# Performance work log

Measured on AMD Instinct MI355X. Metric: run time of the kernel, lower is better.

The kernel has to match this reference:

```python
import jax, jax.numpy as jnp
import numpy as np

L = 1024            # sequence length (env states fed as inputs_embeds)
D_IN = 4            # raw state dim
D_MODEL = 768       # mamba hidden size (mamba-130m-class backbone)
N_LAYERS = 24
D_INNER = 1536      # expand(2) * d_model
D_STATE = 16
D_CONV = 4
DT_RANK = 48        # d_model // 16
EPS = 1e-5


def setup_inputs():
    key = jax.random.key(0)
    ks = jax.random.split(key, 8)
    s = 0.02
    def nrm(k, sh, sc=s):
        return jax.random.normal(k, sh, dtype=jnp.float32) * sc
    # dt bias init: softplus^{-1}(0.01), as in Mamba reference init
    dt_bias = jnp.log(jnp.expm1(jnp.full((N_LAYERS, D_INNER), 0.01, dtype=jnp.float32)))
    # S4D-real init: A_nd = n+1
    A_log = jnp.log(jnp.broadcast_to(jnp.arange(1, D_STATE + 1, dtype=jnp.float32),
                                     (N_LAYERS, D_INNER, D_STATE)))
    return {
        "x": jax.random.normal(ks[0], (L, D_IN), dtype=jnp.float32),
        "w_enc": nrm(ks[1], (D_IN, D_MODEL), 0.5),
        "b_enc": jnp.zeros((D_MODEL,), jnp.float32),
        "norm_w": jnp.ones((N_LAYERS, D_MODEL), jnp.float32),
        "in_proj_w": nrm(ks[2], (N_LAYERS, D_MODEL, 2 * D_INNER)),
        "conv_w": nrm(ks[3], (N_LAYERS, D_INNER, D_CONV), 0.1),
        "conv_b": jnp.zeros((N_LAYERS, D_INNER), jnp.float32),
        "x_proj_w": nrm(ks[4], (N_LAYERS, D_INNER, DT_RANK + 2 * D_STATE)),
        "dt_proj_w": nrm(ks[5], (N_LAYERS, DT_RANK, D_INNER)),
        "dt_proj_b": dt_bias,
        "A_log": A_log,
        "D_skip": jnp.ones((N_LAYERS, D_INNER), jnp.float32),
        "out_proj_w": nrm(ks[6], (N_LAYERS, D_INNER, D_MODEL)),
        "norm_f_w": jnp.ones((D_MODEL,), jnp.float32),
        "fc_w": nrm(ks[7], (D_MODEL, 2), 0.05),
        "fc_b": jnp.zeros((2,), jnp.float32),
    }


def _rmsnorm(x, w):
    return x * jax.lax.rsqrt(jnp.mean(x * x, axis=-1, keepdims=True) + EPS) * w


def _mamba_block(u, p):
    # u: [L, D_MODEL]; pre-norm residual Mamba block
    norm_w, in_w, cw, cb, xp_w, dt_w, dt_b, A_log, D_skip, out_w = p
    h = _rmsnorm(u, norm_w)
    xz = h @ in_w                                   # [L, 2*D_INNER]
    xpart, z = jnp.split(xz, 2, axis=-1)
    # causal depthwise conv1d (kernel D_CONV, left-padded)
    xc = jax.lax.conv_general_dilated(
        xpart.T[None], cw[:, None, :], (1,), [(D_CONV - 1, 0)],
        feature_group_count=D_INNER)[0].T + cb      # [L, D_INNER]
    xc = jax.nn.silu(xc)
    dbl = xc @ xp_w                                 # [L, DT_RANK + 2*D_STATE]
    dt = jax.nn.softplus(dbl[:, :DT_RANK] @ dt_w + dt_b)   # [L, D_INNER]
    B = dbl[:, DT_RANK:DT_RANK + D_STATE]           # [L, D_STATE]
    C = dbl[:, DT_RANK + D_STATE:]                  # [L, D_STATE]
    A = -jnp.exp(A_log)                             # [D_INNER, D_STATE]
    dA = jnp.exp(dt[:, :, None] * A[None])          # [L, D_INNER, D_STATE]
    dBx = dt[:, :, None] * B[:, None, :] * xc[:, :, None]

    def step(hst, t):
        dA_t, dBx_t, C_t = t
        hst = dA_t * hst + dBx_t                    # [D_INNER, D_STATE]
        return hst, hst @ C_t                       # y_t: [D_INNER]

    _, ys = jax.lax.scan(step, jnp.zeros((D_INNER, D_STATE), xc.dtype), (dA, dBx, C))
    y = (ys + D_skip * xc) * jax.nn.silu(z)
    return u + y @ out_w


def reference(x, w_enc, b_enc, norm_w, in_proj_w, conv_w, conv_b, x_proj_w,
              dt_proj_w, dt_proj_b, A_log, D_skip, out_proj_w, norm_f_w, fc_w, fc_b):
    u = x @ w_enc + b_enc                           # state_encoder: [L, D_MODEL]
    params = (norm_w, in_proj_w, conv_w, conv_b, x_proj_w, dt_proj_w,
              dt_proj_b, A_log, D_skip, out_proj_w)
    block = jax.checkpoint(_mamba_block)
    u, _ = jax.lax.scan(lambda c, p: (block(c, p), None), u, params)
    u = _rmsnorm(u, norm_f_w)
    return (u[-1] @ fc_w + fc_b)[None, :]           # logits [1, 2]
```

## Files before the change

### kernel.cpp

```cpp
#include <hip/hip_runtime.h>
#include <hip/hip_bf16.h>

#define L_SEQ 1024
#define D_MODEL 768
#define D_INNER 1536
#define D_STATE 16
#define DT_RANK 48
#define N_LAYERS 24
#define NCHUNK 16
#define CS (L_SEQ / NCHUNK)
#define KSPLIT_OUT 4

typedef __attribute__((ext_vector_type(8))) short short8;
typedef __attribute__((ext_vector_type(4))) float f32x4;

__device__ inline ushort rtn1(float v) {
  unsigned b = __float_as_uint(v);
  return (ushort)((b + 0x7FFF + ((b >> 16) & 1)) >> 16);
}

__device__ inline void gload16(const void* g, void* l) {
  __builtin_amdgcn_global_load_lds(
      (const __attribute__((address_space(1))) void*)g,
      (__attribute__((address_space(3))) void*)l, 16, 0, 0);
}

__global__ __launch_bounds__(256) void tsplit_k(
    const float* __restrict__ in, ushort* __restrict__ hi, int K, int N,
    int Kp) {
  __shared__ float tile[64][65];
  const int l = blockIdx.z;
  const float* src = in + (size_t)l * K * N;
  ushort* dh = hi + (size_t)l * N * Kp;
  const int n0 = blockIdx.x * 64, k0 = blockIdx.y * 64;
  const int tx = threadIdx.x & 63, ty = threadIdx.x >> 6;
#pragma unroll
  for (int rr = 0; rr < 16; rr++) {
    int ky = rr * 4 + ty;
    int k = k0 + ky;
    tile[ky][tx] = (k < K) ? src[(size_t)k * N + n0 + tx] : 0.f;
  }
  __syncthreads();
#pragma unroll
  for (int rr = 0; rr < 16; rr++) {
    int ny = rr * 4 + ty;
    dh[(size_t)(n0 + ny) * Kp + k0 + tx] = rtn1(tile[tx][ny]);
  }
}

template <int EPI>
__global__ __launch_bounds__(256) void gemm_bf16(
    const ushort* __restrict__ A, int lda, const ushort* __restrict__ B,
    int ldb, float* __restrict__ C, int ldc, int K,
    const float* __restrict__ bias) {
  __shared__ ushort lds[2][192 * 32];

  const int tid = threadIdx.x;
  const int bm = blockIdx.y * 128;
  const int bn = blockIdx.x * 64;
  const int kz0 = blockIdx.z * K;
  const int lane = tid & 63;
  const int wid = tid >> 6;
  const int wm = wid & 1, wn = wid >> 1;
  const int r = lane & 15, g = lane >> 4;
  const int segrow = lane >> 2;
  const int segch = lane & 3;

  auto stage = [&](int buf, int k0) {
#pragma unroll
    for (int i = 0; i < 3; i++) {
      int s = wid * 3 + i;
      int gr = s * 16 + segrow;
      int rt = gr & 63;
      int ch = segch ^ ((rt >> 1) & 3);
      bool isA = gr < 128;
      const ushort* src = isA ? A : B;
      int row = isA ? (bm + gr) : (bn + gr - 128);
      int ld = isA ? lda : ldb;
      gload16(src + (size_t)row * ld + k0 + ch * 8, &lds[buf][s * 512]);
    }
  };

  f32x4 acc[4][2] = {};
  const int nt = K / 32;

  stage(0, kz0);

  for (int t = 0; t < nt; t++) {
    const int cur = t & 1;
    if (t + 1 < nt) {
      stage(cur ^ 1, kz0 + (t + 1) * 32);
      asm volatile("s_waitcnt vmcnt(3)" ::: "memory");
    } else {
      asm volatile("s_waitcnt vmcnt(0)" ::: "memory");
    }
    __builtin_amdgcn_s_barrier();
    __builtin_amdgcn_sched_barrier(0);

    short8 af[4], bf[2];
#pragma unroll
    for (int m = 0; m < 4; m++) {
      int row = wm * 64 + m * 16 + r;
      int gg = g ^ ((row >> 1) & 3);
      af[m] = *reinterpret_cast<short8*>(&lds[cur][row * 32 + gg * 8]);
    }
#pragma unroll
    for (int n = 0; n < 2; n++) {
      int row = wn * 32 + n * 16 + r;
      int gg = g ^ ((row >> 1) & 3);
      bf[n] = *reinterpret_cast<short8*>(&lds[cur][(128 + row) * 32 + gg * 8]);
    }
#pragma unroll
    for (int m = 0; m < 4; m++)
#pragma unroll
      for (int n = 0; n < 2; n++)
        acc[m][n] = __builtin_amdgcn_mfma_f32_16x16x32_bf16(
            af[m], bf[n], acc[m][n], 0, 0, 0);
    __builtin_amdgcn_s_barrier();
  }

  float* Cz = C + (size_t)blockIdx.z * gridDim.y * 128 * ldc;
#pragma unroll
  for (int m = 0; m < 4; m++) {
#pragma unroll
    for (int n = 0; n < 2; n++) {
      int row0 = bm + wm * 64 + m * 16 + g * 4;
      int col = bn + wn * 32 + n * 16 + r;
#pragma unroll
      for (int j = 0; j < 4; j++) {
        size_t idx = (size_t)(row0 + j) * ldc + col;
        float v = acc[m][n][j];
        if (EPI == 0) {
          Cz[idx] = v;
        } else {
          v += bias[col];
          Cz[idx] = (v > 20.f) ? v : log1pf(__expf(v));
        }
      }
    }
  }
}

__global__ __launch_bounds__(256) void encode_k(
    const float* __restrict__ x, const float* __restrict__ w_enc,
    const float* __restrict__ b_enc, float* __restrict__ u) {
  int d = blockIdx.x * 256 + threadIdx.x;
  int t = blockIdx.y;
  const float4 xv = *(const float4*)(x + t * 4);
  float acc = b_enc[d];
  acc = fmaf(xv.x, w_enc[0 * D_MODEL + d], acc);
  acc = fmaf(xv.y, w_enc[1 * D_MODEL + d], acc);
  acc = fmaf(xv.z, w_enc[2 * D_MODEL + d], acc);
  acc = fmaf(xv.w, w_enc[3 * D_MODEL + d], acc);
  u[t * D_MODEL + d] = acc;
}

__global__ __launch_bounds__(256) void rmsnorm_b_k(
    const float* __restrict__ u, const float* __restrict__ w,
    ushort* __restrict__ hb) {
  int t = blockIdx.x;
  const float* ur = u + t * D_MODEL;
  float ss = 0.f;
  float vl[3];
#pragma unroll
  for (int p = 0; p < 3; p++) {
    int d = threadIdx.x + p * 256;
    vl[p] = ur[d];
    ss = fmaf(vl[p], vl[p], ss);
  }
#pragma unroll
  for (int o = 1; o < 64; o <<= 1) ss += __shfl_xor(ss, o);
  __shared__ float red[4];
  int wid = threadIdx.x >> 6;
  if ((threadIdx.x & 63) == 0) red[wid] = ss;
  __syncthreads();
  float rs = rsqrtf((red[0] + red[1] + red[2] + red[3]) / (float)D_MODEL +
                    1e-5f);
#pragma unroll
  for (int p = 0; p < 3; p++) {
    int d = threadIdx.x + p * 256;
    hb[t * D_MODEL + d] = rtn1(vl[p] * rs * w[d]);
  }
}

__global__ __launch_bounds__(256) void rmsnorm_add_k(
    const float* __restrict__ Po, float* __restrict__ u,
    const float* __restrict__ w, ushort* __restrict__ hb) {
  int t = blockIdx.x;
  float* ur = u + t * D_MODEL;
  float ss = 0.f;
  float vl[3];
#pragma unroll
  for (int p = 0; p < 3; p++) {
    int d = threadIdx.x + p * 256;
    float v = ur[d];
#pragma unroll
    for (int z = 0; z < KSPLIT_OUT; z++)
      v += Po[(size_t)z * L_SEQ * D_MODEL + (size_t)t * D_MODEL + d];
    ur[d] = v;
    vl[p] = v;
    ss = fmaf(v, v, ss);
  }
#pragma unroll
  for (int o = 1; o < 64; o <<= 1) ss += __shfl_xor(ss, o);
  __shared__ float red[4];
  int wid = threadIdx.x >> 6;
  if ((threadIdx.x & 63) == 0) red[wid] = ss;
  __syncthreads();
  float rs = rsqrtf((red[0] + red[1] + red[2] + red[3]) / (float)D_MODEL +
                    1e-5f);
#pragma unroll
  for (int p = 0; p < 3; p++) {
    int d = threadIdx.x + p * 256;
    hb[t * D_MODEL + d] = rtn1(vl[p] * rs * w[d]);
  }
}

#define DBL_NS 8
#define DBL_KSEG (D_INNER / DBL_NS)
__global__ __launch_bounds__(256) void gemm_dblconv_k(
    const float* __restrict__ xz, const float* __restrict__ cw,
    const float* __restrict__ cb, const float* __restrict__ B,
    float* __restrict__ P, float* __restrict__ xc) {
  __shared__ float As2[16][17];
  __shared__ float Bs2[16][80];
  const int tid = threadIdx.x;
  const int bm = blockIdx.y * 16;
  const int ks0 = blockIdx.x * DBL_KSEG;
  const int tx = tid % 16;
  const int ty = tid / 16;
  const int sm = tid / 16, sk = tid % 16;
  const int t = bm + sm;

  float4 wv;
  float cbv, xv0, xv1, xv2, xv3, bv0, bv1, bv2, bv3, bv4;
  auto issue = [&](int k0) {
    int c = k0 + sk;
    wv = *(const float4*)(cw + c * 4);
    cbv = cb[c];
    xv0 = (t >= 3) ? xz[(size_t)(t - 3) * 2 * D_INNER + c] : 0.f;
    xv1 = (t >= 2) ? xz[(size_t)(t - 2) * 2 * D_INNER + c] : 0.f;
    xv2 = (t >= 1) ? xz[(size_t)(t - 1) * 2 * D_INNER + c] : 0.f;
    xv3 = xz[(size_t)t * 2 * D_INNER + c];
    bv0 = B[(size_t)(k0 + (tid + 0) / 80) * 80 + (tid + 0) % 80];
    bv1 = B[(size_t)(k0 + (tid + 256) / 80) * 80 + (tid + 256) % 80];
    bv2 = B[(size_t)(k0 + (tid + 512) / 80) * 80 + (tid + 512) % 80];
    bv3 = B[(size_t)(k0 + (tid + 768) / 80) * 80 + (tid + 768) % 80];
    bv4 = B[(size_t)(k0 + (tid + 1024) / 80) * 80 + (tid + 1024) % 80];
  };

  float acc[5] = {0.f, 0.f, 0.f, 0.f, 0.f};

  issue(ks0);

  for (int k0 = ks0; k0 < ks0 + DBL_KSEG; k0 += 16) {
    float a = cbv;
    a = fmaf(xv0, wv.x, a);
    a = fmaf(xv1, wv.y, a);
    a = fmaf(xv2, wv.z, a);
    a = fmaf(xv3, wv.w, a);
    float v = a / (1.f + __expf(-a));
    xc[(size_t)t * D_INNER + k0 + sk] = v;
    As2[sk][sm] = v;
    Bs2[(tid + 0) / 80][(tid + 0) % 80] = bv0;
    Bs2[(tid + 256) / 80][(tid + 256) % 80] = bv1;
    Bs2[(tid + 512) / 80][(tid + 512) % 80] = bv2;
    Bs2[(tid + 768) / 80][(tid + 768) % 80] = bv3;
    Bs2[(tid + 1024) / 80][(tid + 1024) % 80] = bv4;
    if (k0 + 16 < ks0 + DBL_KSEG) issue(k0 + 16);
    asm volatile("s_waitcnt lgkmcnt(0)" ::: "memory");
    __builtin_amdgcn_s_barrier();
    __builtin_amdgcn_sched_barrier(0);
#pragma unroll
    for (int k = 0; k < 16; k++) {
      float ra = As2[k][ty];
#pragma unroll
      for (int j = 0; j < 5; j++) acc[j] = fmaf(ra, Bs2[k][tx * 5 + j], acc[j]);
    }
    __builtin_amdgcn_s_barrier();
  }

  float* p = P + ((size_t)blockIdx.x * L_SEQ + bm + ty) * 80 + tx * 5;
#pragma unroll
  for (int j = 0; j < 5; j++) p[j] = acc[j];
}

__global__ __launch_bounds__(256) void dbl_reduce_k(
    const float* __restrict__ P, float* __restrict__ dbl,
    ushort* __restrict__ dab) {
  int i = blockIdx.x * 256 + threadIdx.x;
  float s = 0.f;
#pragma unroll
  for (int ks = 0; ks < DBL_NS; ks++) s += P[(size_t)ks * L_SEQ * 80 + i];
  dbl[i] = s;
  int rowi = i / 80, col = i % 80;
  if (col < DT_RANK) {
    dab[rowi * 64 + col] = rtn1(s);
  } else if (col >= 64) {
    dab[rowi * 64 + col - 16] = 0;
  }
}

__global__ __launch_bounds__(256) void scan1_k(
    const float* __restrict__ dt, const float* __restrict__ xc,
    const float* __restrict__ dbl, const float* __restrict__ A_log,
    float* __restrict__ Pb, float* __restrict__ Eb) {
  __shared__ float s_dt[CS][16];
  __shared__ float s_xc[CS][16];
  __shared__ float s_b[CS][16];
  const int tid = threadIdx.x;
  const int s = tid & 15;
  const int cl = tid >> 4;
  const int c0 = blockIdx.y * 16;
  const int c = c0 + cl;
  const int t0 = blockIdx.x * CS;
  const float a = -__expf(A_log[c * D_STATE + s]);

  const int lc = tid & 15, lt = tid >> 4;
#pragma unroll
  for (int p = 0; p < CS / 16; p++) {
    int t = lt + p * 16;
    size_t gt = (size_t)(t0 + t);
    s_dt[t][lc] = dt[gt * D_INNER + c0 + lc];
    s_xc[t][lc] = xc[gt * D_INNER + c0 + lc];
    s_b[t][lc] = dbl[gt * 80 + DT_RANK + lc];
  }
  __syncthreads();

  float P = 1.f, h = 0.f;
  for (int t = 0; t < CS; t++) {
    float dtv = s_dt[t][cl];
    float dA = __expf(dtv * a);
    P *= dA;
    h = fmaf(dA, h, dtv * s_b[t][s] * s_xc[t][cl]);
  }
  int idx = blockIdx.x * (D_INNER * D_STATE) + c0 * D_STATE + tid;
  Pb[idx] = P;
  Eb[idx] = h;
}

__global__ __launch_bounds__(256) void scan3_k(
    const float* __restrict__ dt, const float* __restrict__ xc,
    const float* __restrict__ dbl, const float* __restrict__ xz,
    const float* __restrict__ A_log, const float* __restrict__ D_skip,
    const float* __restrict__ Pb, const float* __restrict__ Eb,
    ushort* __restrict__ yb16) {
  __shared__ float s_dt[CS][16];
  __shared__ float s_xc[CS][16];
  __shared__ float s_z[CS][16];
  __shared__ float s_bc[CS][32];

  const int tid = threadIdx.x;
  const int s = tid & 15;
  const int cl = tid >> 4;
  const int c0 = blockIdx.y * 16;
  const int c = c0 + cl;
  const int t0 = blockIdx.x * CS;

  const float a = -__expf(A_log[c * D_STATE + s]);
  const float Dv = D_skip[c];

  const int lc = tid & 15, lt = tid >> 4;
  const int bj = tid & 31, bt = tid >> 5;
#pragma unroll
  for (int p = 0; p < CS / 16; p++) {
    int t = lt + p * 16;
    size_t gt = (size_t)(t0 + t);
    s_dt[t][lc] = dt[gt * D_INNER + c0 + lc];
    s_xc[t][lc] = xc[gt * D_INNER + c0 + lc];
    s_z[t][lc] = xz[gt * 2 * D_INNER + D_INNER + c0 + lc];
  }
#pragma unroll
  for (int p = 0; p < CS / 8; p++) {
    int t = bt + p * 8;
    s_bc[t][bj] = dbl[(size_t)(t0 + t) * 80 + DT_RANK + bj];
  }

  float hst = 0.f;
  {
    const int nj = blockIdx.x;
    const int base = c0 * D_STATE + tid;
    float pj[NCHUNK - 1], ej[NCHUNK - 1];
#pragma unroll
    for (int jj = 0; jj < NCHUNK - 1; jj++) {
      if (jj < nj) {
        int o = jj * (D_INNER * D_STATE) + base;
        pj[jj] = Pb[o];
        ej[jj] = Eb[o];
      }
    }
#pragma unroll
    for (int jj = 0; jj < NCHUNK - 1; jj++)
      if (jj < nj) hst = fmaf(pj[jj], hst, ej[jj]);
  }
  __syncthreads();

  for (int t = 0; t < CS; t++) {
    float dtv = s_dt[t][cl];
    float xv = s_xc[t][cl];
    float Bv = s_bc[t][s];
    float Cv = s_bc[t][16 + s];
    float dA = __expf(dtv * a);
    hst = fmaf(dA, hst, dtv * Bv * xv);
    float p2 = hst * Cv;
    p2 += __shfl_xor(p2, 1);
    p2 += __shfl_xor(p2, 2);
    p2 += __shfl_xor(p2, 4);
    p2 += __shfl_xor(p2, 8);
    if (s == 0) {
      float zv = s_z[t][cl];
      float sz = zv / (1.f + __expf(-zv));
      yb16[(size_t)(t0 + t) * D_INNER + c] = rtn1((p2 + Dv * xv) * sz);
    }
  }
}

__global__ __launch_bounds__(256) void final_k(
    const float* __restrict__ u, const float* __restrict__ Po,
    const float* __restrict__ nfw, const float* __restrict__ fcw,
    const float* __restrict__ fcb, float* __restrict__ out) {
  const float* ur = u + (size_t)(L_SEQ - 1) * D_MODEL;
  float ss = 0.f;
  float vl[3];
#pragma unroll
  for (int p = 0; p < 3; p++) {
    int d = threadIdx.x + p * 256;
    float v = ur[d];
#pragma unroll
    for (int z = 0; z < KSPLIT_OUT; z++)
      v += Po[(size_t)z * L_SEQ * D_MODEL + (size_t)(L_SEQ - 1) * D_MODEL + d];
    vl[p] = v;
    ss = fmaf(v, v, ss);
  }
#pragma unroll
  for (int o = 1; o < 64; o <<= 1) ss += __shfl_xor(ss, o);
  __shared__ float red[4];
  int wid = threadIdx.x >> 6;
  if ((threadIdx.x & 63) == 0) red[wid] = ss;
  __syncthreads();
  float rs = rsqrtf((red[0] + red[1] + red[2] + red[3]) / (float)D_MODEL +
                    1e-5f);
  float a0 = 0.f, a1 = 0.f;
#pragma unroll
  for (int p = 0; p < 3; p++) {
    int d = threadIdx.x + p * 256;
    float hn = vl[p] * rs * nfw[d];
    a0 = fmaf(hn, fcw[d * 2 + 0], a0);
    a1 = fmaf(hn, fcw[d * 2 + 1], a1);
  }
#pragma unroll
  for (int o = 1; o < 64; o <<= 1) {
    a0 += __shfl_xor(a0, o);
    a1 += __shfl_xor(a1, o);
  }
  __shared__ float r0[4], r1[4];
  if ((threadIdx.x & 63) == 0) {
    r0[wid] = a0;
    r1[wid] = a1;
  }
  __syncthreads();
  if (threadIdx.x == 0) out[0] = r0[0] + r0[1] + r0[2] + r0[3] + fcb[0];
  if (threadIdx.x == 1) out[1] = r1[0] + r1[1] + r1[2] + r1[3] + fcb[1];
}

extern "C" void kernel_launch(void* const* d_in, const int* in_sizes, int n_in,
                              void* d_out, int out_size, void* d_ws,
                              size_t ws_size, hipStream_t stream) {
  const float* x      = (const float*)d_in[0];
  const float* w_enc  = (const float*)d_in[1];
  const float* b_enc  = (const float*)d_in[2];
  const float* norm_w = (const float*)d_in[3];
  const float* in_w   = (const float*)d_in[4];
  const float* conv_w = (const float*)d_in[5];
  const float* conv_b = (const float*)d_in[6];
  const float* xp_w   = (const float*)d_in[7];
  const float* dt_w   = (const float*)d_in[8];
  const float* dt_b   = (const float*)d_in[9];
  const float* A_log  = (const float*)d_in[10];
  const float* D_skip = (const float*)d_in[11];
  const float* out_w  = (const float*)d_in[12];
  const float* nf_w   = (const float*)d_in[13];
  const float* fc_w   = (const float*)d_in[14];
  const float* fc_b   = (const float*)d_in[15];
  float* out = (float*)d_out;

  float* u   = (float*)d_ws;
  float* xzb = u   + (size_t)L_SEQ * D_MODEL;
  float* xcb = xzb + (size_t)L_SEQ * 2 * D_INNER;
  float* dbl = xcb + (size_t)L_SEQ * D_INNER;
  float* dtb = dbl + (size_t)L_SEQ * 80;
  float* yb  = dtb + (size_t)L_SEQ * D_INNER;
  float* Po  = yb  + (size_t)L_SEQ * 80 * DBL_NS;
  float* Pb  = Po  + (size_t)KSPLIT_OUT * L_SEQ * D_MODEL;
  float* Eb  = Pb  + (size_t)NCHUNK * D_INNER * D_STATE;
  float* fend = Eb + (size_t)NCHUNK * D_INNER * D_STATE;

  ushort* hb   = (ushort*)fend;
  ushort* dab  = hb + (size_t)L_SEQ * D_MODEL;
  ushort* yb16 = dab + (size_t)L_SEQ * 64;
  ushort* wxT  = yb16 + (size_t)L_SEQ * D_INNER;
  ushort* wdT  = wxT + (size_t)N_LAYERS * 2 * D_INNER * D_MODEL;
  ushort* woT  = wdT + (size_t)N_LAYERS * D_INNER * 64;

  tsplit_k<<<dim3(2 * D_INNER / 64, D_MODEL / 64, N_LAYERS), 256, 0, stream>>>(
      in_w, wxT, D_MODEL, 2 * D_INNER, D_MODEL);
  tsplit_k<<<dim3(D_INNER / 64, 1, N_LAYERS), 256, 0, stream>>>(
      dt_w, wdT, DT_RANK, D_INNER, 64);
  tsplit_k<<<dim3(D_MODEL / 64, D_INNER / 64, N_LAYERS), 256, 0, stream>>>(
      out_w, woT, D_INNER, D_MODEL, D_INNER);

  encode_k<<<dim3(3, L_SEQ), 256, 0, stream>>>(x, w_enc, b_enc, u);

  for (int l = 0; l < N_LAYERS; l++) {
    const float* cw_l    = conv_w + (size_t)l * D_INNER * 4;
    const float* cb_l    = conv_b + (size_t)l * D_INNER;
    const float* xp_w_l  = xp_w  + (size_t)l * D_INNER * 80;
    const float* dt_b_l  = dt_b  + (size_t)l * D_INNER;
    const float* A_log_l = A_log + (size_t)l * D_INNER * D_STATE;
    const float* D_l     = D_skip + (size_t)l * D_INNER;
    const ushort* wxT_l = wxT + (size_t)l * 2 * D_INNER * D_MODEL;
    const ushort* wdT_l = wdT + (size_t)l * D_INNER * 64;
    const ushort* woT_l = woT + (size_t)l * D_MODEL * D_INNER;

    if (l == 0) {
      rmsnorm_b_k<<<L_SEQ, 256, 0, stream>>>(
          u, norm_w + (size_t)l * D_MODEL, hb);
    } else {
      rmsnorm_add_k<<<L_SEQ, 256, 0, stream>>>(
          Po, u, norm_w + (size_t)l * D_MODEL, hb);
    }
    gemm_bf16<0><<<dim3(2 * D_INNER / 64, L_SEQ / 128), 256, 0, stream>>>(
        hb, D_MODEL, wxT_l, D_MODEL, xzb, 2 * D_INNER, D_MODEL, nullptr);
    gemm_dblconv_k<<<dim3(DBL_NS, L_SEQ / 16), 256, 0, stream>>>(
        xzb, cw_l, cb_l, xp_w_l, yb, xcb);
    dbl_reduce_k<<<(L_SEQ * 80) / 256, 256, 0, stream>>>(yb, dbl, dab);
    gemm_bf16<1><<<dim3(D_INNER / 64, L_SEQ / 128), 256, 0, stream>>>(
        dab, 64, wdT_l, 64, dtb, D_INNER, 64, dt_b_l);
    scan1_k<<<dim3(NCHUNK, D_INNER / 16), 256, 0, stream>>>(
        dtb, xcb, dbl, A_log_l, Pb, Eb);
    scan3_k<<<dim3(NCHUNK, D_INNER / 16), 256, 0, stream>>>(
        dtb, xcb, dbl, xzb, A_log_l, D_l, Pb, Eb, yb16);
    gemm_bf16<0><<<dim3(D_MODEL / 64, L_SEQ / 128, KSPLIT_OUT), 256, 0,
                   stream>>>(yb16, D_INNER, woT_l, D_INNER, Po, D_MODEL,
                             D_INNER / KSPLIT_OUT, nullptr);
  }

  final_k<<<1, 256, 0, stream>>>(u, Po, nf_w, fc_w, fc_b, out);
}
```

Baseline: 2.680 ms.

## Fuse x_proj, split-K reduce and dt_proj into one kernel per row block

Replaces the split-K x_proj GEMM, its reduction kernel and the bf16 dt_proj GEMM with one kernel per 16-row block. That kernel computes conv+SiLU and x_proj over the full inner dimension, then dt_proj with softplus in fp32 from shared memory. This removes two launches per layer, the partial-sum buffer and the dt weight transpose, and the weight transpose kernel now writes packed 32-bit pairs. In exchange, the fused kernel launches only 64 blocks, each with a long serial K loop and scalar fp32 work, which sharply reduces parallelism.

```diff
diff --git a/kernel.cpp b/kernel.cpp
--- a/kernel.cpp
+++ b/kernel.cpp
@@ -41,18 +41,20 @@
     tile[ky][tx] = (k < K) ? src[(size_t)k * N + n0 + tx] : 0.f;
   }
   __syncthreads();
-#pragma unroll
-  for (int rr = 0; rr < 16; rr++) {
-    int ny = rr * 4 + ty;
-    dh[(size_t)(n0 + ny) * Kp + k0 + tx] = rtn1(tile[tx][ny]);
-  }
-}
-
-template <int EPI>
+  const int txk = threadIdx.x & 31;
+  const int tyn = threadIdx.x >> 5;
+#pragma unroll
+  for (int rr = 0; rr < 8; rr++) {
+    int ny = rr * 8 + tyn;
+    unsigned p = (unsigned)rtn1(tile[2 * txk][ny]) |
+                 ((unsigned)rtn1(tile[2 * txk + 1][ny]) << 16);
+    *(unsigned*)&dh[(size_t)(n0 + ny) * Kp + k0 + 2 * txk] = p;
+  }
+}
+
 __global__ __launch_bounds__(256) void gemm_bf16(
     const ushort* __restrict__ A, int lda, const ushort* __restrict__ B,
-    int ldb, float* __restrict__ C, int ldc, int K,
-    const float* __restrict__ bias) {
+    int ldb, float* __restrict__ C, int ldc, int K) {
   __shared__ ushort lds[2][192 * 32];
 
   const int tid = threadIdx.x;
@@ -127,16 +129,8 @@
       int row0 = bm + wm * 64 + m * 16 + g * 4;
       int col = bn + wn * 32 + n * 16 + r;
 #pragma unroll
-      for (int j = 0; j < 4; j++) {
-        size_t idx = (size_t)(row0 + j) * ldc + col;
-        float v = acc[m][n][j];
-        if (EPI == 0) {
-          Cz[idx] = v;
-        } else {
-          v += bias[col];
-          Cz[idx] = (v > 20.f) ? v : log1pf(__expf(v));
-        }
-      }
+      for (int j = 0; j < 4; j++)
+        Cz[(size_t)(row0 + j) * ldc + col] = acc[m][n][j];
     }
   }
 }
@@ -216,17 +210,20 @@
   }
 }
 
-#define DBL_NS 8
-#define DBL_KSEG (D_INNER / DBL_NS)
-__global__ __launch_bounds__(256) void gemm_dblconv_k(
+#define DTW_CHUNK 256
+__global__ __launch_bounds__(256) void dblconv_dt_k(
     const float* __restrict__ xz, const float* __restrict__ cw,
     const float* __restrict__ cb, const float* __restrict__ B,
-    float* __restrict__ P, float* __restrict__ xc) {
+    const float* __restrict__ dtw, const float* __restrict__ dtbias,
+    float* __restrict__ dbl, float* __restrict__ xc,
+    float* __restrict__ dtb) {
   __shared__ float As2[16][17];
   __shared__ float Bs2[16][80];
+  __shared__ float s_dbl[16][48];
+  __shared__ float wch[48][DTW_CHUNK + 1];
+
   const int tid = threadIdx.x;
-  const int bm = blockIdx.y * 16;
-  const int ks0 = blockIdx.x * DBL_KSEG;
+  const int bm = blockIdx.x * 16;
   const int tx = tid % 16;
   const int ty = tid / 16;
   const int sm = tid / 16, sk = tid % 16;
@@ -251,9 +248,9 @@
 
   float acc[5] = {0.f, 0.f, 0.f, 0.f, 0.f};
 
-  issue(ks0);
-
-  for (int k0 = ks0; k0 < ks0 + DBL_KSEG; k0 += 16) {
+  issue(0);
+
+  for (int k0 = 0; k0 < D_INNER; k0 += 16) {
     float a = cbv;
     a = fmaf(xv0, wv.x, a);
     a = fmaf(xv1, wv.y, a);
@@ -267,7 +264,7 @@
     Bs2[(tid + 512) / 80][(tid + 512) % 80] = bv2;
     Bs2[(tid + 768) / 80][(tid + 768) % 80] = bv3;
     Bs2[(tid + 1024) / 80][(tid + 1024) % 80] = bv4;
-    if (k0 + 16 < ks0 + DBL_KSEG) issue(k0 + 16);
+    if (k0 + 16 < D_INNER) issue(k0 + 16);
     asm volatile("s_waitcnt lgkmcnt(0)" ::: "memory");
     __builtin_amdgcn_s_barrier();
     __builtin_amdgcn_sched_barrier(0);
@@ -280,24 +277,33 @@
     __builtin_amdgcn_s_barrier();
   }
 
-  float* p = P + ((size_t)blockIdx.x * L_SEQ + bm + ty) * 80 + tx * 5;
-#pragma unroll
-  for (int j = 0; j < 5; j++) p[j] = acc[j];
-}
-
-__global__ __launch_bounds__(256) void dbl_reduce_k(
-    const float* __restrict__ P, float* __restrict__ dbl,
-    ushort* __restrict__ dab) {
-  int i = blockIdx.x * 256 + threadIdx.x;
-  float s = 0.f;
-#pragma unroll
-  for (int ks = 0; ks < DBL_NS; ks++) s += P[(size_t)ks * L_SEQ * 80 + i];
-  dbl[i] = s;
-  int rowi = i / 80, col = i % 80;
-  if (col < DT_RANK) {
-    dab[rowi * 64 + col] = rtn1(s);
-  } else if (col >= 64) {
-    dab[rowi * 64 + col - 16] = 0;
+  float* dr = dbl + (size_t)(bm + ty) * 80 + tx * 5;
+#pragma unroll
+  for (int j = 0; j < 5; j++) {
+    dr[j] = acc[j];
+    int c = tx * 5 + j;
+    if (c < DT_RANK) s_dbl[ty][c] = acc[j];
+  }
+
+  const int row = tid >> 4;
+  const int cl = tid & 15;
+  for (int cc = 0; cc < D_INNER; cc += DTW_CHUNK) {
+    __syncthreads();
+    for (int i = tid; i < DT_RANK * DTW_CHUNK; i += 256) {
+      int j = i / DTW_CHUNK, c = i % DTW_CHUNK;
+      wch[j][c] = dtw[(size_t)j * D_INNER + cc + c];
+    }
+    __syncthreads();
+#pragma unroll
+    for (int i = 0; i < DTW_CHUNK / 16; i++) {
+      int c = cl + i * 16;
+      float s = dtbias[cc + c];
+#pragma unroll
+      for (int j = 0; j < DT_RANK; j++)
+        s = fmaf(s_dbl[row][j], wch[j][c], s);
+      float sp = (s > 20.f) ? s : log1pf(__expf(s));
+      dtb[(size_t)(bm + row) * D_INNER + cc + c] = sp;
+    }
   }
 }
 
@@ -489,23 +495,18 @@
   float* xcb = xzb + (size_t)L_SEQ * 2 * D_INNER;
   float* dbl = xcb + (size_t)L_SEQ * D_INNER;
   float* dtb = dbl + (size_t)L_SEQ * 80;
-  float* yb  = dtb + (size_t)L_SEQ * D_INNER;
-  float* Po  = yb  + (size_t)L_SEQ * 80 * DBL_NS;
+  float* Po  = dtb + (size_t)L_SEQ * D_INNER;
   float* Pb  = Po  + (size_t)KSPLIT_OUT * L_SEQ * D_MODEL;
   float* Eb  = Pb  + (size_t)NCHUNK * D_INNER * D_STATE;
   float* fend = Eb + (size_t)NCHUNK * D_INNER * D_STATE;
 
   ushort* hb   = (ushort*)fend;
-  ushort* dab  = hb + (size_t)L_SEQ * D_MODEL;
-  ushort* yb16 = dab + (size_t)L_SEQ * 64;
+  ushort* yb16 = hb + (size_t)L_SEQ * D_MODEL;
   ushort* wxT  = yb16 + (size_t)L_SEQ * D_INNER;
-  ushort* wdT  = wxT + (size_t)N_LAYERS * 2 * D_INNER * D_MODEL;
-  ushort* woT  = wdT + (size_t)N_LAYERS * D_INNER * 64;
+  ushort* woT  = wxT + (size_t)N_LAYERS * 2 * D_INNER * D_MODEL;
 
   tsplit_k<<<dim3(2 * D_INNER / 64, D_MODEL / 64, N_LAYERS), 256, 0, stream>>>(
       in_w, wxT, D_MODEL, 2 * D_INNER, D_MODEL);
-  tsplit_k<<<dim3(D_INNER / 64, 1, N_LAYERS), 256, 0, stream>>>(
-      dt_w, wdT, DT_RANK, D_INNER, 64);
   tsplit_k<<<dim3(D_MODEL / 64, D_INNER / 64, N_LAYERS), 256, 0, stream>>>(
       out_w, woT, D_INNER, D_MODEL, D_INNER);
 
@@ -515,11 +516,11 @@
     const float* cw_l    = conv_w + (size_t)l * D_INNER * 4;
     const float* cb_l    = conv_b + (size_t)l * D_INNER;
     const float* xp_w_l  = xp_w  + (size_t)l * D_INNER * 80;
+    const float* dt_w_l  = dt_w  + (size_t)l * DT_RANK * D_INNER;
     const float* dt_b_l  = dt_b  + (size_t)l * D_INNER;
     const float* A_log_l = A_log + (size_t)l * D_INNER * D_STATE;
     const float* D_l     = D_skip + (size_t)l * D_INNER;
     const ushort* wxT_l = wxT + (size_t)l * 2 * D_INNER * D_MODEL;
-    const ushort* wdT_l = wdT + (size_t)l * D_INNER * 64;
     const ushort* woT_l = woT + (size_t)l * D_MODEL * D_INNER;
 
     if (l == 0) {
@@ -529,20 +530,17 @@
       rmsnorm_add_k<<<L_SEQ, 256, 0, stream>>>(
           Po, u, norm_w + (size_t)l * D_MODEL, hb);
     }
-    gemm_bf16<0><<<dim3(2 * D_INNER / 64, L_SEQ / 128), 256, 0, stream>>>(
-        hb, D_MODEL, wxT_l, D_MODEL, xzb, 2 * D_INNER, D_MODEL, nullptr);
-    gemm_dblconv_k<<<dim3(DBL_NS, L_SEQ / 16), 256, 0, stream>>>(
-        xzb, cw_l, cb_l, xp_w_l, yb, xcb);
-    dbl_reduce_k<<<(L_SEQ * 80) / 256, 256, 0, stream>>>(yb, dbl, dab);
-    gemm_bf16<1><<<dim3(D_INNER / 64, L_SEQ / 128), 256, 0, stream>>>(
-        dab, 64, wdT_l, 64, dtb, D_INNER, 64, dt_b_l);
+    gemm_bf16<<<dim3(2 * D_INNER / 64, L_SEQ / 128), 256, 0, stream>>>(
+        hb, D_MODEL, wxT_l, D_MODEL, xzb, 2 * D_INNER, D_MODEL);
+    dblconv_dt_k<<<L_SEQ / 16, 256, 0, stream>>>(
+        xzb, cw_l, cb_l, xp_w_l, dt_w_l, dt_b_l, dbl, xcb, dtb);
     scan1_k<<<dim3(NCHUNK, D_INNER / 16), 256, 0, stream>>>(
         dtb, xcb, dbl, A_log_l, Pb, Eb);
     scan3_k<<<dim3(NCHUNK, D_INNER / 16), 256, 0, stream>>>(
         dtb, xcb, dbl, xzb, A_log_l, D_l, Pb, Eb, yb16);
-    gemm_bf16<0><<<dim3(D_MODEL / 64, L_SEQ / 128, KSPLIT_OUT), 256, 0,
-                   stream>>>(yb16, D_INNER, woT_l, D_INNER, Po, D_MODEL,
-                             D_INNER / KSPLIT_OUT, nullptr);
+    gemm_bf16<<<dim3(D_MODEL / 64, L_SEQ / 128, KSPLIT_OUT), 256, 0,
+                stream>>>(yb16, D_INNER, woT_l, D_INNER, Po, D_MODEL,
+                          D_INNER / KSPLIT_OUT);
   }
 
   final_k<<<1, 256, 0, stream>>>(u, Po, nf_w, fc_w, fc_b, out);
```

Measured after the change: 5.494 ms. +105.0%, slower.
